# Performance work log

Measured on AMD Instinct MI355X. Metric: run time of the kernel, lower is better.

Reference implementation:

```python
import jax, jax.numpy as jnp
import numpy as np

BLOCK_SPLIT = (4, 4, 4)
GRID = 256
N_BLOCK = 64
BX = GRID // 4  # 64, per-block grid resolution along each axis
N_PTS = 4_194_304


def setup_inputs() -> dict:
    key = jax.random.key(0)
    k1, k2 = jax.random.split(key)
    aabb = jnp.array([[-1.5, -1.5, -1.5], [1.5, 1.5, 1.5]], dtype=jnp.float32)
    # points roughly inside the aabb
    xyz_sampled = jax.random.uniform(k1, (N_PTS, 3), dtype=jnp.float32) * 3.0 - 1.5
    alpha_volume = jax.random.uniform(k2, (GRID, GRID, GRID), dtype=jnp.float32)
    # per-block domains (as kilonerf global_to_local expects): block AABBs
    idx = np.stack(np.meshgrid(np.arange(4), np.arange(4), np.arange(4), indexing='ij'), -1).reshape(-1, 3)
    voxel = np.array([3.0 / 4.0] * 3)
    dmin = (-1.5 + idx * voxel).astype(np.float32)
    dmax = (dmin + voxel).astype(np.float32)
    return {"xyz_sampled": xyz_sampled, "aabb": aabb, "alpha_volume": alpha_volume,
            "domain_min": jnp.asarray(dmin), "domain_max": jnp.asarray(dmax)}


def _sample_alpha(xyz, aabb, alpha_volume, dmin, dmax):
    bs = jnp.asarray(BLOCK_SPLIT, jnp.float32)
    voxel = (aabb[1] - aabb[0]) / bs                      # per-block world size
    idx3 = jnp.floor((xyz - aabb[0]) / voxel).astype(jnp.int32)
    idx3 = jnp.clip(idx3, 0, jnp.array(BLOCK_SPLIT, jnp.int32) - 1)  # edge clamp (matches loop)
    strides = jnp.array([BLOCK_SPLIT[2] * BLOCK_SPLIT[1], BLOCK_SPLIT[2], 1], jnp.int32)
    bid = (idx3 * strides).sum(-1)                        # [N] block id in [0, 64)

    order = jnp.argsort(bid)                              # jax sort is stable; matches bucket-by-block order
    bid_s = bid[order]
    pts = xyz[order]

    # global_to_local (kilonerf): map into per-block [-1,1]^3
    local = 2.0 * (pts - dmin[bid_s]) / (dmax[bid_s] - dmin[bid_s]) - 1.0  # [N,3] (gx,gy,gz)

    # torch .view(64,1,64,64,64) is a raw contiguous reinterpretation -> plain reshape
    vols = alpha_volume.reshape(N_BLOCK, BX, BX, BX)      # [B, D, H, W]
    D = H = W = BX
    # grid_sample convention: grid x -> W axis, y -> H axis, z -> D axis; align_corners=True
    fx = (local[:, 0] + 1.0) * 0.5 * (W - 1)
    fy = (local[:, 1] + 1.0) * 0.5 * (H - 1)
    fz = (local[:, 2] + 1.0) * 0.5 * (D - 1)
    x0 = jnp.floor(fx); y0 = jnp.floor(fy); z0 = jnp.floor(fz)
    wx = fx - x0; wy = fy - y0; wz = fz - z0
    x0i = x0.astype(jnp.int32); y0i = y0.astype(jnp.int32); z0i = z0.astype(jnp.int32)

    def fetch(zi, yi, xi):
        # zeros padding for out-of-range corners (grid_sample padding_mode='zeros')
        inb = (zi >= 0) & (zi < D) & (yi >= 0) & (yi < H) & (xi >= 0) & (xi < W)
        v = vols[bid_s, jnp.clip(zi, 0, D - 1), jnp.clip(yi, 0, H - 1), jnp.clip(xi, 0, W - 1)]
        return jnp.where(inb, v, 0.0)

    out = jnp.zeros_like(fx)
    for dz, wz_ in ((0, 1.0 - wz), (1, wz)):
        for dy, wy_ in ((0, 1.0 - wy), (1, wy)):
            for dx, wx_ in ((0, 1.0 - wx), (1, wx)):
                out = out + wz_ * wy_ * wx_ * fetch(z0i + dz, y0i + dy, x0i + dx)
    return out  # [N] alpha values in block-sorted order


def reference(xyz_sampled, aabb, alpha_volume, domain_min, domain_max):
    return _sample_alpha(xyz_sampled, aabb, alpha_volume, domain_min, domain_max)
```

## Files before the change

### kernel.cpp

```cpp
#include <hip/hip_runtime.h>

#define NB     64
#define NF     4096
#define TILE   16384
#define HBLK   1024
#define DBLK   1024
#define FBLK   512
#define GBLK   256
#define SBLK   256
#define FB_TILE 4096
#define STAGE_HALF 8192

__device__ __forceinline__ int compute_bid(float px, float py, float pz,
                                           float a0x, float a0y, float a0z,
                                           float vx, float vy, float vz) {
    int ix = (int)floorf((px - a0x) / vx);
    int iy = (int)floorf((py - a0y) / vy);
    int iz = (int)floorf((pz - a0z) / vz);
    ix = min(max(ix, 0), 3);
    iy = min(max(iy, 0), 3);
    iz = min(max(iz, 0), 3);
    return ix * 16 + iy * 4 + iz;
}

__device__ __forceinline__ void quant_point(float px, float py, float pz,
        float a0x, float a0y, float a0z, float vx, float vy, float vz,
        const float* s_dn, const float* s_sc,
        int& b, int& qx, int& qy, int& qz, int& key) {
    b = compute_bid(px, py, pz, a0x, a0y, a0z, vx, vy, vz);
    float fx = (px - s_dn[3 * b])     * s_sc[3 * b];
    float fy = (py - s_dn[3 * b + 1]) * s_sc[3 * b + 1];
    float fz = (pz - s_dn[3 * b + 2]) * s_sc[3 * b + 2];
    qx = min(max(__float2int_rn(fx * 256.0f), 0), 16128);
    qy = min(max(__float2int_rn(fy * 256.0f), 0), 16128);
    qz = min(max(__float2int_rn(fz * 256.0f), 0), 16128);
    key = (b << 6) | ((qz >> 12) << 4) | ((qy >> 12) << 2) | (qx >> 12);
}

__global__ void __launch_bounds__(HBLK) hist_kernel(
        const float* __restrict__ xyz, const float* __restrict__ aabb,
        const float* __restrict__ dmin, const float* __restrict__ dmax,
        int* __restrict__ hist64, int* __restrict__ tot4096, int N, int T) {
    __shared__ int   sh[NF];
    __shared__ float s_dn[192], s_sc[192];
    const int tid = threadIdx.x, g = blockIdx.x;
    for (int l = tid; l < NF; l += HBLK) sh[l] = 0;
    if (tid < 192) { s_dn[tid] = dmin[tid]; s_sc[tid] = 63.0f / (dmax[tid] - dmin[tid]); }
    const float a0x = aabb[0], a0y = aabb[1], a0z = aabb[2];
    const float vx = (aabb[3] - a0x) * 0.25f;
    const float vy = (aabb[4] - a0y) * 0.25f;
    const float vz = (aabb[5] - a0z) * 0.25f;
    __syncthreads();
    for (int c = 0; c < TILE / (HBLK * 4); ++c) {
        int p0 = g * TILE + c * (HBLK * 4) + tid * 4;
        int b, qx, qy, qz, k;
        if (p0 + 3 < N) {
            const float4* v4 = (const float4*)(xyz + (size_t)p0 * 3);
            float4 f0 = v4[0], f1 = v4[1], f2 = v4[2];
            quant_point(f0.x, f0.y, f0.z, a0x, a0y, a0z, vx, vy, vz, s_dn, s_sc, b, qx, qy, qz, k);
            atomicAdd(&sh[k], 1);
            quant_point(f0.w, f1.x, f1.y, a0x, a0y, a0z, vx, vy, vz, s_dn, s_sc, b, qx, qy, qz, k);
            atomicAdd(&sh[k], 1);
            quant_point(f1.z, f1.w, f2.x, a0x, a0y, a0z, vx, vy, vz, s_dn, s_sc, b, qx, qy, qz, k);
            atomicAdd(&sh[k], 1);
            quant_point(f2.y, f2.z, f2.w, a0x, a0y, a0z, vx, vy, vz, s_dn, s_sc, b, qx, qy, qz, k);
            atomicAdd(&sh[k], 1);
        } else {
            for (int t = 0; t < 4; ++t) {
                int i = p0 + t;
                if (i < N) {
                    quant_point(xyz[3 * i], xyz[3 * i + 1], xyz[3 * i + 2],
                                a0x, a0y, a0z, vx, vy, vz, s_dn, s_sc, b, qx, qy, qz, k);
                    atomicAdd(&sh[k], 1);
                }
            }
        }
    }
    __syncthreads();
    for (int l = tid; l < NF; l += HBLK) {
        int c = sh[l];
        if (c) atomicAdd(&tot4096[l], c);
    }
    if (tid < NB) {
        int s = 0;
        #pragma unroll
        for (int j = 0; j < 64; ++j) s += sh[tid * 64 + j];
        hist64[tid * T + g] = s;
    }
}

__global__ void scans_kernel(int* __restrict__ hist64, int* __restrict__ tot64,
                             const int* __restrict__ tot4096,
                             int* __restrict__ foff, int* __restrict__ fcnt, int G) {
    __shared__ int sh[SBLK];
    const int t = threadIdx.x;
    if (blockIdx.x < NB) {
        const int b = blockIdx.x;
        const int L = (G + SBLK - 1) / SBLK;
        const int lo = t * L;
        const int n = min(L, max(0, G - lo));
        const int base = b * G + lo;
        int s = 0;
        for (int k = 0; k < n; ++k) s += hist64[base + k];
        sh[t] = s;
        __syncthreads();
        for (int off = 1; off < SBLK; off <<= 1) {
            int v = (t >= off) ? sh[t - off] : 0;
            __syncthreads();
            sh[t] += v;
            __syncthreads();
        }
        int excl = (t == 0) ? 0 : sh[t - 1];
        for (int k = 0; k < n; ++k) {
            int v = hist64[base + k];
            hist64[base + k] = excl;
            excl += v;
        }
        if (t == SBLK - 1) tot64[b] = sh[SBLK - 1];
    } else {
        const int L = NF / SBLK;
        int loc[16];
        int s = 0;
        #pragma unroll
        for (int j = 0; j < L; ++j) { loc[j] = tot4096[t * L + j]; s += loc[j]; }
        sh[t] = s;
        __syncthreads();
        for (int o = 1; o < SBLK; o <<= 1) {
            int v = (t >= o) ? sh[t - o] : 0;
            __syncthreads();
            sh[t] += v;
            __syncthreads();
        }
        int run = (t == 0) ? 0 : sh[t - 1];
        #pragma unroll
        for (int j = 0; j < L; ++j) {
            foff[t * L + j] = run;
            fcnt[t * L + j] = run;
            run += loc[j];
        }
        if (t == SBLK - 1) foff[NF] = run;
    }
}

__global__ void __launch_bounds__(DBLK) scatterC_kernel(
        const float* __restrict__ xyz, const float* __restrict__ aabb,
        const float* __restrict__ dmin, const float* __restrict__ dmax,
        const int* __restrict__ hist64, const int* __restrict__ tot64,
        unsigned long long* __restrict__ payloadC, int N, int T) {
    __shared__ unsigned long long stage[STAGE_HALF];
    __shared__ int   s_wh[16][NB];
    __shared__ int   s_cnt0[NB];
    __shared__ int   s_off[NB];
    __shared__ int   s_start[NB];
    __shared__ int   s_gb[NB];
    __shared__ float s_dn[192], s_sc[192];
    const int tid = threadIdx.x, g = blockIdx.x;
    const int lane = tid & 63, wv = tid >> 6;
    if (tid < NB) s_off[tid] = tot64[tid];
    if (tid < 192) { s_dn[tid] = dmin[tid]; s_sc[tid] = 63.0f / (dmax[tid] - dmin[tid]); }
    ((int*)s_wh)[tid] = 0;
    const float a0x = aabb[0], a0y = aabb[1], a0z = aabb[2];
    const float vx = (aabb[3] - a0x) * 0.25f;
    const float vy = (aabb[4] - a0y) * 0.25f;
    const float vz = (aabb[5] - a0z) * 0.25f;
    __syncthreads();
    for (int o = 1; o < NB; o <<= 1) {
        int v = (tid < NB && tid >= o) ? s_off[tid - o] : 0;
        __syncthreads();
        if (tid < NB) s_off[tid] += v;
        __syncthreads();
    }
    if (tid < NB) s_cnt0[tid] = hist64[tid * T + g] + (tid ? s_off[tid - 1] : 0);

    const unsigned long long lt = (1ull << lane) - 1ull;
    const int base_i = g * TILE + wv * 1024;
    unsigned long long cache[16];
    #pragma unroll
    for (int r = 0; r < 16; ++r) {
        int i = base_i + r * 64 + lane;
        bool valid = (i < N);
        int b = 0, qx = 0, qy = 0, qz = 0, key;
        if (valid) {
            quant_point(xyz[3 * i], xyz[3 * i + 1], xyz[3 * i + 2],
                        a0x, a0y, a0z, vx, vy, vz, s_dn, s_sc, b, qx, qy, qz, key);
        }
        unsigned long long m = __ballot(valid);
        #pragma unroll
        for (int q = 0; q < 6; ++q) {
            unsigned long long bal = __ballot((b >> q) & 1);
            m &= ((b >> q) & 1) ? bal : ~bal;
        }
        int rank = __popcll(m & lt);
        int run = valid ? s_wh[wv][b] : 0;
        if (valid && rank == 0) s_wh[wv][b] = run + __popcll(m);
        int localpos = run + rank;
        cache[r] = (unsigned long long)(unsigned)qx
                 | ((unsigned long long)(unsigned)qy << 14)
                 | ((unsigned long long)(unsigned)qz << 28)
                 | ((unsigned long long)(unsigned)b  << 42)
                 | ((unsigned long long)(unsigned)localpos << 48);
    }
    __syncthreads();
    for (int o = 1; o < 16; o <<= 1) {
        int v = (wv >= o) ? s_wh[wv - o][lane] : 0;
        __syncthreads();
        s_wh[wv][lane] += v;
        __syncthreads();
    }
    if (wv == 0) {
        int v = s_wh[15][lane];
        int incl = v;
        #pragma unroll
        for (int o = 1; o < 64; o <<= 1) {
            int u = __shfl_up(incl, o);
            if (lane >= o) incl += u;
        }
        int excl = incl - v;
        s_start[lane] = excl;
        s_gb[lane] = s_cnt0[lane] - excl;
    }
    __syncthreads();
    const int n = min(TILE, N - g * TILE);
    #pragma unroll
    for (int r = 0; r < 16; ++r) {
        int i = base_i + r * 64 + lane;
        if (i < N) {
            unsigned long long cc = cache[r];
            int b = (int)((cc >> 42) & 63);
            int localpos = (int)((cc >> 48) & 1023);
            int lidx = s_start[b] + (wv ? s_wh[wv - 1][b] : 0) + localpos;
            unsigned long long p48 = cc & ((1ull << 48) - 1);
            if (lidx < STAGE_HALF) stage[lidx] = p48;
            cache[r] = p48 | ((unsigned long long)(unsigned)lidx << 48);
        }
    }
    __syncthreads();
    {
        int nA = min(n, STAGE_HALF);
        for (int j = tid; j < nA; j += DBLK) {
            unsigned long long p = stage[j];
            int b = (int)((p >> 42) & 63);
            payloadC[s_gb[b] + j] = p;
        }
    }
    __syncthreads();
    #pragma unroll
    for (int r = 0; r < 16; ++r) {
        int i = base_i + r * 64 + lane;
        if (i < N) {
            unsigned long long cc = cache[r];
            int lidx = (int)(cc >> 48);
            if (lidx >= STAGE_HALF)
                stage[lidx - STAGE_HALF] = cc & ((1ull << 48) - 1);
        }
    }
    __syncthreads();
    for (int j = STAGE_HALF + tid; j < n; j += DBLK) {
        unsigned long long p = stage[j - STAGE_HALF];
        int b = (int)((p >> 42) & 63);
        payloadC[s_gb[b] + j] = p;
    }
}

__global__ void __launch_bounds__(FBLK) scatterF_kernel(
        const unsigned long long* __restrict__ payloadC,
        int* __restrict__ fcnt,
        unsigned long long* __restrict__ payloadF, int N) {
    __shared__ int s_fb[NF];
    const int tid = threadIdx.x, t2 = blockIdx.x;
    for (int l = tid; l < NF; l += FBLK) s_fb[l] = 0;
    __syncthreads();
    const int lo = t2 * TILE;
    const int n = min(TILE, N - lo);
    for (int j = tid; j < n; j += FBLK) {
        unsigned long long p = payloadC[lo + j];
        int qx = (int)(p & 16383), qy = (int)((p >> 14) & 16383);
        int qz = (int)((p >> 28) & 16383), b = (int)((p >> 42) & 63);
        int key = (b << 6) | ((qz >> 12) << 4) | ((qy >> 12) << 2) | (qx >> 12);
        atomicAdd(&s_fb[key], 1);
    }
    __syncthreads();
    for (int l = tid; l < NF; l += FBLK) {
        int c = s_fb[l];
        s_fb[l] = c ? atomicAdd(&fcnt[l], c) : 0;
    }
    __syncthreads();
    for (int j = tid; j < n; j += FBLK) {
        unsigned long long p = payloadC[lo + j];
        int qx = (int)(p & 16383), qy = (int)((p >> 14) & 16383);
        int qz = (int)((p >> 28) & 16383), b = (int)((p >> 42) & 63);
        int key = (b << 6) | ((qz >> 12) << 4) | ((qy >> 12) << 2) | (qx >> 12);
        int fpos = atomicAdd(&s_fb[key], 1);
        payloadF[fpos] = (p & ((1ull << 42) - 1))
                       | ((unsigned long long)(unsigned)(lo + j) << 42);
    }
}

__global__ void __launch_bounds__(GBLK) gather_kernel(
        const float* __restrict__ vol,
        const unsigned long long* __restrict__ payloadF,
        const int* __restrict__ foff, float* __restrict__ out) {
    __shared__ float sv[17 * 17 * 17];
    const int tid = threadIdx.x;
    const int nb = gridDim.x, d = blockIdx.x;
    const int k = (nb % 8 == 0) ? (d % 8) * (nb / 8) + (d / 8) : d;
    const int b = k >> 6;
    const int bz = ((k >> 4) & 3) * 16, by = ((k >> 2) & 3) * 16, bx = (k & 3) * 16;
    const float* vb = vol + ((size_t)b << 18);
    for (int l = tid; l < 17 * 17 * 17; l += GBLK) {
        int z = l / 289, r = l - z * 289, y = r / 17, x = r - y * 17;
        int gz = bz + z, gy = by + y, gx = bx + x;
        sv[l] = (gz < 64 && gy < 64 && gx < 64)
                    ? vb[(gz << 12) + (gy << 6) + gx] : 0.0f;
    }
    __syncthreads();
    const int lo = foff[k];
    const int n = foff[k + 1] - lo;
    for (int j = tid; j < n; j += GBLK) {
        unsigned long long p = payloadF[lo + j];
        int qx = (int)(p & 16383), qy = (int)((p >> 14) & 16383);
        int qz = (int)((p >> 28) & 16383);
        int pos = (int)(p >> 42);
        float wx = (qx & 255) * (1.0f / 256.0f);
        float wy = (qy & 255) * (1.0f / 256.0f);
        float wz = (qz & 255) * (1.0f / 256.0f);
        int lx = (qx >> 8) - bx, ly = (qy >> 8) - by, lz = (qz >> 8) - bz;
        int base = lz * 289 + ly * 17 + lx;
        float v000 = sv[base],       v001 = sv[base + 1];
        float v010 = sv[base + 17],  v011 = sv[base + 18];
        float v100 = sv[base + 289], v101 = sv[base + 290];
        float v110 = sv[base + 306], v111 = sv[base + 307];
        float c00 = v000 + wx * (v001 - v000);
        float c01 = v010 + wx * (v011 - v010);
        float c10 = v100 + wx * (v101 - v100);
        float c11 = v110 + wx * (v111 - v110);
        float c0 = c00 + wy * (c01 - c00);
        float c1 = c10 + wy * (c11 - c10);
        out[pos] = c0 + wz * (c1 - c0);
    }
}

__global__ void fb_hist_kernel(const float* __restrict__ xyz,
                               const float* __restrict__ aabb,
                               int* __restrict__ hist, int N, int G) {
    __shared__ int s_h[NB];
    const int tid = threadIdx.x, g = blockIdx.x;
    if (tid < NB) s_h[tid] = 0;
    __syncthreads();
    const float a0x = aabb[0], a0y = aabb[1], a0z = aabb[2];
    const float vx = (aabb[3] - a0x) * 0.25f;
    const float vy = (aabb[4] - a0y) * 0.25f;
    const float vz = (aabb[5] - a0z) * 0.25f;
    for (int c = 0; c < FB_TILE / 256; ++c) {
        int i = g * FB_TILE + c * 256 + tid;
        if (i < N)
            atomicAdd(&s_h[compute_bid(xyz[3 * i], xyz[3 * i + 1], xyz[3 * i + 2],
                                       a0x, a0y, a0z, vx, vy, vz)], 1);
    }
    __syncthreads();
    if (tid < NB) hist[tid * G + g] = s_h[tid];
}

__global__ void fb_scan_kernel(int* __restrict__ hist, int* __restrict__ tot, int G) {
    __shared__ int sh[SBLK];
    const int b = blockIdx.x, t = threadIdx.x;
    const int L = (G + SBLK - 1) / SBLK;
    const int lo = t * L;
    const int n = min(L, max(0, G - lo));
    const int base = b * G + lo;
    int s = 0;
    for (int k = 0; k < n; ++k) s += hist[base + k];
    sh[t] = s;
    __syncthreads();
    for (int off = 1; off < SBLK; off <<= 1) {
        int v = (t >= off) ? sh[t - off] : 0;
        __syncthreads();
        sh[t] += v;
        __syncthreads();
    }
    int excl = (t == 0) ? 0 : sh[t - 1];
    for (int k = 0; k < n; ++k) {
        int v = hist[base + k];
        hist[base + k] = excl;
        excl += v;
    }
    if (t == SBLK - 1) tot[b] = sh[SBLK - 1];
}

__global__ void fb_scatter_kernel(const float* __restrict__ xyz,
                                  const float* __restrict__ aabb,
                                  const float* __restrict__ dmin,
                                  const float* __restrict__ dmax,
                                  const float* __restrict__ vol,
                                  const int* __restrict__ hist,
                                  const int* __restrict__ tot64,
                                  float* __restrict__ out, int N, int G) {
    __shared__ int   s_cnt[NB], s_off[NB];
    __shared__ int   s_whist[4][NB];
    __shared__ float s_dn[192], s_sc[192];
    const int tid = threadIdx.x, g = blockIdx.x;
    if (tid < NB) s_off[tid] = tot64[tid];
    if (tid < 192) { s_dn[tid] = dmin[tid]; s_sc[tid] = 63.0f / (dmax[tid] - dmin[tid]); }
    __syncthreads();
    for (int o = 1; o < NB; o <<= 1) {
        int v = (tid < NB && tid >= o) ? s_off[tid - o] : 0;
        __syncthreads();
        if (tid < NB) s_off[tid] += v;
        __syncthreads();
    }
    if (tid < NB) s_cnt[tid] = hist[tid * G + g] + (tid ? s_off[tid - 1] : 0);
    const float a0x = aabb[0], a0y = aabb[1], a0z = aabb[2];
    const float vx = (aabb[3] - a0x) * 0.25f;
    const float vy = (aabb[4] - a0y) * 0.25f;
    const float vz = (aabb[5] - a0z) * 0.25f;
    __syncthreads();
    const int lane = tid & 63, wv = tid >> 6;
    const unsigned long long lt = (1ull << lane) - 1ull;
    for (int c = 0; c < FB_TILE / 256; ++c) {
        int i = g * FB_TILE + c * 256 + tid;
        bool valid = (i < N);
        int b = 0;
        float alpha = 0.0f;
        if (valid) {
            float px = xyz[3 * i], py = xyz[3 * i + 1], pz = xyz[3 * i + 2];
            b = compute_bid(px, py, pz, a0x, a0y, a0z, vx, vy, vz);
            float fx = (px - s_dn[3 * b])     * s_sc[3 * b];
            float fy = (py - s_dn[3 * b + 1]) * s_sc[3 * b + 1];
            float fz = (pz - s_dn[3 * b + 2]) * s_sc[3 * b + 2];
            float x0f = floorf(fx), y0f = floorf(fy), z0f = floorf(fz);
            float wx = fx - x0f, wy = fy - y0f, wz = fz - z0f;
            int x0 = (int)x0f, y0 = (int)y0f, z0 = (int)z0f;
            const float* vb = vol + ((size_t)b << 18);
            auto F = [&](int zi, int yi, int xi) -> float {
                if ((unsigned)zi >= 64u || (unsigned)yi >= 64u || (unsigned)xi >= 64u)
                    return 0.0f;
                return vb[(zi << 12) + (yi << 6) + xi];
            };
            float s = 0.0f;
            s += (1.0f - wz) * (1.0f - wy) * (1.0f - wx) * F(z0,     y0,     x0);
            s += (1.0f - wz) * (1.0f - wy) * wx          * F(z0,     y0,     x0 + 1);
            s += (1.0f - wz) * wy          * (1.0f - wx) * F(z0,     y0 + 1, x0);
            s += (1.0f - wz) * wy          * wx          * F(z0,     y0 + 1, x0 + 1);
            s += wz          * (1.0f - wy) * (1.0f - wx) * F(z0 + 1, y0,     x0);
            s += wz          * (1.0f - wy) * wx          * F(z0 + 1, y0,     x0 + 1);
            s += wz          * wy          * (1.0f - wx) * F(z0 + 1, y0 + 1, x0);
            s += wz          * wy          * wx          * F(z0 + 1, y0 + 1, x0 + 1);
            alpha = s;
        }
        ((int*)s_whist)[tid] = 0;
        __syncthreads();
        unsigned long long m = __ballot(valid);
        #pragma unroll
        for (int q = 0; q < 6; ++q) {
            unsigned long long bal = __ballot((b >> q) & 1);
            m &= ((b >> q) & 1) ? bal : ~bal;
        }
        int rank = __popcll(m & lt);
        if (valid && rank == 0) s_whist[wv][b] = __popcll(m);
        __syncthreads();
        if (valid) {
            int pos = s_cnt[b] + rank;
            for (int w2 = 0; w2 < wv; ++w2) pos += s_whist[w2][b];
            out[pos] = alpha;
        }
        __syncthreads();
        if (tid < NB)
            s_cnt[tid] += s_whist[0][tid] + s_whist[1][tid] +
                          s_whist[2][tid] + s_whist[3][tid];
        __syncthreads();
    }
}

extern "C" void kernel_launch(void* const* d_in, const int* in_sizes, int n_in,
                              void* d_out, int out_size, void* d_ws, size_t ws_size,
                              hipStream_t stream) {
    const float* xyz  = (const float*)d_in[0];
    const float* aabb = (const float*)d_in[1];
    const float* vol  = (const float*)d_in[2];
    const float* dmin = (const float*)d_in[3];
    const float* dmax = (const float*)d_in[4];
    float* out = (float*)d_out;
    const int N = in_sizes[0] / 3;
    const int T = (N + TILE - 1) / TILE;

    auto align = [](size_t x) { return (x + 255) & ~(size_t)255; };
    char* ws = (char*)d_ws;
    size_t o = 0;
    unsigned long long* payloadC = (unsigned long long*)(ws + o); o += align((size_t)N * 8);
    unsigned long long* payloadF = (unsigned long long*)(ws + o); o += align((size_t)N * 8);
    int* hist64  = (int*)(ws + o); o += align((size_t)NB * T * 4);
    int* tot64   = (int*)(ws + o); o += 256;
    int* tot4096 = (int*)(ws + o); o += align((size_t)NF * 4);
    int* foff    = (int*)(ws + o); o += align((size_t)(NF + 1) * 4);
    int* fcnt    = (int*)(ws + o); o += align((size_t)NF * 4);
    const bool fine = (N <= (1 << 22)) && (ws_size >= o);

    if (fine) {
        hipMemsetAsync(tot4096, 0, NF * 4, stream);
        hist_kernel<<<T, HBLK, 0, stream>>>(xyz, aabb, dmin, dmax,
                                            hist64, tot4096, N, T);
        scans_kernel<<<NB + 1, SBLK, 0, stream>>>(hist64, tot64, tot4096,
                                                  foff, fcnt, T);
        scatterC_kernel<<<T, DBLK, 0, stream>>>(xyz, aabb, dmin, dmax,
                                                hist64, tot64, payloadC, N, T);
        scatterF_kernel<<<T, FBLK, 0, stream>>>(payloadC, fcnt, payloadF, N);
        gather_kernel<<<NF, GBLK, 0, stream>>>(vol, payloadF, foff, out);
    } else {
        const int Gf = (N + FB_TILE - 1) / FB_TILE;
        int* h = (int*)ws;
        int* t = (int*)(ws + align((size_t)NB * Gf * 4));
        fb_hist_kernel<<<Gf, 256, 0, stream>>>(xyz, aabb, h, N, Gf);
        fb_scan_kernel<<<NB, SBLK, 0, stream>>>(h, t, Gf);
        fb_scatter_kernel<<<Gf, 256, 0, stream>>>(xyz, aabb, dmin, dmax, vol,
                                                  h, t, out, N, Gf);
    }
}
```

Before: 256.6 us.

## Drop fine-grained sub-block sort and gather directly from block-sorted payload

Removes the 4096-bucket fine histogram, its scan, the second scatter pass (scatterF) and the LDS-staged sub-block gather. Instead the gather kernel reads the block-sorted payloadC in output order and does eight trilinear loads straight from the global volume, writing coalesced outputs. This cuts a full read/write pass over N 8-byte payloads plus the extra atomics and memset. In exchange, volume reads lose the shared-memory tile reuse and rely on L2/cache locality within each 64^3 block (1 MB per block).

```diff
diff --git a/kernel.cpp b/kernel.cpp
--- a/kernel.cpp
+++ b/kernel.cpp
@@ -1,12 +1,11 @@
 #include <hip/hip_runtime.h>
 
 #define NB     64
-#define NF     4096
 #define TILE   16384
 #define HBLK   1024
 #define DBLK   1024
-#define FBLK   512
-#define GBLK   256
+#define GDBLK  256
+#define GDPTS  4096
 #define SBLK   256
 #define FB_TILE 4096
 #define STAGE_HALF 8192
@@ -26,7 +25,7 @@
 __device__ __forceinline__ void quant_point(float px, float py, float pz,
         float a0x, float a0y, float a0z, float vx, float vy, float vz,
         const float* s_dn, const float* s_sc,
-        int& b, int& qx, int& qy, int& qz, int& key) {
+        int& b, int& qx, int& qy, int& qz) {
     b = compute_bid(px, py, pz, a0x, a0y, a0z, vx, vy, vz);
     float fx = (px - s_dn[3 * b])     * s_sc[3 * b];
     float fy = (py - s_dn[3 * b + 1]) * s_sc[3 * b + 1];
@@ -34,18 +33,14 @@
     qx = min(max(__float2int_rn(fx * 256.0f), 0), 16128);
     qy = min(max(__float2int_rn(fy * 256.0f), 0), 16128);
     qz = min(max(__float2int_rn(fz * 256.0f), 0), 16128);
-    key = (b << 6) | ((qz >> 12) << 4) | ((qy >> 12) << 2) | (qx >> 12);
 }
 
 __global__ void __launch_bounds__(HBLK) hist_kernel(
         const float* __restrict__ xyz, const float* __restrict__ aabb,
-        const float* __restrict__ dmin, const float* __restrict__ dmax,
-        int* __restrict__ hist64, int* __restrict__ tot4096, int N, int T) {
-    __shared__ int   sh[NF];
-    __shared__ float s_dn[192], s_sc[192];
+        int* __restrict__ hist64, int N, int T) {
+    __shared__ int s_h[NB];
     const int tid = threadIdx.x, g = blockIdx.x;
-    for (int l = tid; l < NF; l += HBLK) sh[l] = 0;
-    if (tid < 192) { s_dn[tid] = dmin[tid]; s_sc[tid] = 63.0f / (dmax[tid] - dmin[tid]); }
+    if (tid < NB) s_h[tid] = 0;
     const float a0x = aabb[0], a0y = aabb[1], a0z = aabb[2];
     const float vx = (aabb[3] - a0x) * 0.25f;
     const float vy = (aabb[4] - a0y) * 0.25f;
@@ -53,93 +48,51 @@
     __syncthreads();
     for (int c = 0; c < TILE / (HBLK * 4); ++c) {
         int p0 = g * TILE + c * (HBLK * 4) + tid * 4;
-        int b, qx, qy, qz, k;
         if (p0 + 3 < N) {
             const float4* v4 = (const float4*)(xyz + (size_t)p0 * 3);
             float4 f0 = v4[0], f1 = v4[1], f2 = v4[2];
-            quant_point(f0.x, f0.y, f0.z, a0x, a0y, a0z, vx, vy, vz, s_dn, s_sc, b, qx, qy, qz, k);
-            atomicAdd(&sh[k], 1);
-            quant_point(f0.w, f1.x, f1.y, a0x, a0y, a0z, vx, vy, vz, s_dn, s_sc, b, qx, qy, qz, k);
-            atomicAdd(&sh[k], 1);
-            quant_point(f1.z, f1.w, f2.x, a0x, a0y, a0z, vx, vy, vz, s_dn, s_sc, b, qx, qy, qz, k);
-            atomicAdd(&sh[k], 1);
-            quant_point(f2.y, f2.z, f2.w, a0x, a0y, a0z, vx, vy, vz, s_dn, s_sc, b, qx, qy, qz, k);
-            atomicAdd(&sh[k], 1);
+            atomicAdd(&s_h[compute_bid(f0.x, f0.y, f0.z, a0x, a0y, a0z, vx, vy, vz)], 1);
+            atomicAdd(&s_h[compute_bid(f0.w, f1.x, f1.y, a0x, a0y, a0z, vx, vy, vz)], 1);
+            atomicAdd(&s_h[compute_bid(f1.z, f1.w, f2.x, a0x, a0y, a0z, vx, vy, vz)], 1);
+            atomicAdd(&s_h[compute_bid(f2.y, f2.z, f2.w, a0x, a0y, a0z, vx, vy, vz)], 1);
         } else {
             for (int t = 0; t < 4; ++t) {
                 int i = p0 + t;
-                if (i < N) {
-                    quant_point(xyz[3 * i], xyz[3 * i + 1], xyz[3 * i + 2],
-                                a0x, a0y, a0z, vx, vy, vz, s_dn, s_sc, b, qx, qy, qz, k);
-                    atomicAdd(&sh[k], 1);
-                }
+                if (i < N)
+                    atomicAdd(&s_h[compute_bid(xyz[3 * i], xyz[3 * i + 1],
+                                               xyz[3 * i + 2],
+                                               a0x, a0y, a0z, vx, vy, vz)], 1);
             }
         }
     }
     __syncthreads();
-    for (int l = tid; l < NF; l += HBLK) {
-        int c = sh[l];
-        if (c) atomicAdd(&tot4096[l], c);
-    }
-    if (tid < NB) {
-        int s = 0;
-        #pragma unroll
-        for (int j = 0; j < 64; ++j) s += sh[tid * 64 + j];
-        hist64[tid * T + g] = s;
-    }
-}
-
-__global__ void scans_kernel(int* __restrict__ hist64, int* __restrict__ tot64,
-                             const int* __restrict__ tot4096,
-                             int* __restrict__ foff, int* __restrict__ fcnt, int G) {
+    if (tid < NB) hist64[tid * T + g] = s_h[tid];
+}
+
+__global__ void fb_scan_kernel(int* __restrict__ hist, int* __restrict__ tot, int G) {
     __shared__ int sh[SBLK];
-    const int t = threadIdx.x;
-    if (blockIdx.x < NB) {
-        const int b = blockIdx.x;
-        const int L = (G + SBLK - 1) / SBLK;
-        const int lo = t * L;
-        const int n = min(L, max(0, G - lo));
-        const int base = b * G + lo;
-        int s = 0;
-        for (int k = 0; k < n; ++k) s += hist64[base + k];
-        sh[t] = s;
-        __syncthreads();
-        for (int off = 1; off < SBLK; off <<= 1) {
-            int v = (t >= off) ? sh[t - off] : 0;
-            __syncthreads();
-            sh[t] += v;
-            __syncthreads();
-        }
-        int excl = (t == 0) ? 0 : sh[t - 1];
-        for (int k = 0; k < n; ++k) {
-            int v = hist64[base + k];
-            hist64[base + k] = excl;
-            excl += v;
-        }
-        if (t == SBLK - 1) tot64[b] = sh[SBLK - 1];
-    } else {
-        const int L = NF / SBLK;
-        int loc[16];
-        int s = 0;
-        #pragma unroll
-        for (int j = 0; j < L; ++j) { loc[j] = tot4096[t * L + j]; s += loc[j]; }
-        sh[t] = s;
-        __syncthreads();
-        for (int o = 1; o < SBLK; o <<= 1) {
-            int v = (t >= o) ? sh[t - o] : 0;
-            __syncthreads();
-            sh[t] += v;
-            __syncthreads();
-        }
-        int run = (t == 0) ? 0 : sh[t - 1];
-        #pragma unroll
-        for (int j = 0; j < L; ++j) {
-            foff[t * L + j] = run;
-            fcnt[t * L + j] = run;
-            run += loc[j];
-        }
-        if (t == SBLK - 1) foff[NF] = run;
-    }
+    const int b = blockIdx.x, t = threadIdx.x;
+    const int L = (G + SBLK - 1) / SBLK;
+    const int lo = t * L;
+    const int n = min(L, max(0, G - lo));
+    const int base = b * G + lo;
+    int s = 0;
+    for (int k = 0; k < n; ++k) s += hist[base + k];
+    sh[t] = s;
+    __syncthreads();
+    for (int off = 1; off < SBLK; off <<= 1) {
+        int v = (t >= off) ? sh[t - off] : 0;
+        __syncthreads();
+        sh[t] += v;
+        __syncthreads();
+    }
+    int excl = (t == 0) ? 0 : sh[t - 1];
+    for (int k = 0; k < n; ++k) {
+        int v = hist[base + k];
+        hist[base + k] = excl;
+        excl += v;
+    }
+    if (t == SBLK - 1) tot[b] = sh[SBLK - 1];
 }
 
 __global__ void __launch_bounds__(DBLK) scatterC_kernel(
@@ -179,10 +132,10 @@
     for (int r = 0; r < 16; ++r) {
         int i = base_i + r * 64 + lane;
         bool valid = (i < N);
-        int b = 0, qx = 0, qy = 0, qz = 0, key;
+        int b = 0, qx = 0, qy = 0, qz = 0;
         if (valid) {
             quant_point(xyz[3 * i], xyz[3 * i + 1], xyz[3 * i + 2],
-                        a0x, a0y, a0z, vx, vy, vz, s_dn, s_sc, b, qx, qy, qz, key);
+                        a0x, a0y, a0z, vx, vy, vz, s_dn, s_sc, b, qx, qy, qz);
         }
         unsigned long long m = __ballot(valid);
         #pragma unroll
@@ -262,81 +215,38 @@
     }
 }
 
-__global__ void __launch_bounds__(FBLK) scatterF_kernel(
+__global__ void __launch_bounds__(GDBLK) gather_kernel(
+        const float* __restrict__ vol,
         const unsigned long long* __restrict__ payloadC,
-        int* __restrict__ fcnt,
-        unsigned long long* __restrict__ payloadF, int N) {
-    __shared__ int s_fb[NF];
-    const int tid = threadIdx.x, t2 = blockIdx.x;
-    for (int l = tid; l < NF; l += FBLK) s_fb[l] = 0;
-    __syncthreads();
-    const int lo = t2 * TILE;
-    const int n = min(TILE, N - lo);
-    for (int j = tid; j < n; j += FBLK) {
-        unsigned long long p = payloadC[lo + j];
-        int qx = (int)(p & 16383), qy = (int)((p >> 14) & 16383);
-        int qz = (int)((p >> 28) & 16383), b = (int)((p >> 42) & 63);
-        int key = (b << 6) | ((qz >> 12) << 4) | ((qy >> 12) << 2) | (qx >> 12);
-        atomicAdd(&s_fb[key], 1);
-    }
-    __syncthreads();
-    for (int l = tid; l < NF; l += FBLK) {
-        int c = s_fb[l];
-        s_fb[l] = c ? atomicAdd(&fcnt[l], c) : 0;
-    }
-    __syncthreads();
-    for (int j = tid; j < n; j += FBLK) {
-        unsigned long long p = payloadC[lo + j];
-        int qx = (int)(p & 16383), qy = (int)((p >> 14) & 16383);
-        int qz = (int)((p >> 28) & 16383), b = (int)((p >> 42) & 63);
-        int key = (b << 6) | ((qz >> 12) << 4) | ((qy >> 12) << 2) | (qx >> 12);
-        int fpos = atomicAdd(&s_fb[key], 1);
-        payloadF[fpos] = (p & ((1ull << 42) - 1))
-                       | ((unsigned long long)(unsigned)(lo + j) << 42);
-    }
-}
-
-__global__ void __launch_bounds__(GBLK) gather_kernel(
-        const float* __restrict__ vol,
-        const unsigned long long* __restrict__ payloadF,
-        const int* __restrict__ foff, float* __restrict__ out) {
-    __shared__ float sv[17 * 17 * 17];
-    const int tid = threadIdx.x;
+        float* __restrict__ out, int N) {
     const int nb = gridDim.x, d = blockIdx.x;
-    const int k = (nb % 8 == 0) ? (d % 8) * (nb / 8) + (d / 8) : d;
-    const int b = k >> 6;
-    const int bz = ((k >> 4) & 3) * 16, by = ((k >> 2) & 3) * 16, bx = (k & 3) * 16;
-    const float* vb = vol + ((size_t)b << 18);
-    for (int l = tid; l < 17 * 17 * 17; l += GBLK) {
-        int z = l / 289, r = l - z * 289, y = r / 17, x = r - y * 17;
-        int gz = bz + z, gy = by + y, gx = bx + x;
-        sv[l] = (gz < 64 && gy < 64 && gx < 64)
-                    ? vb[(gz << 12) + (gy << 6) + gx] : 0.0f;
-    }
-    __syncthreads();
-    const int lo = foff[k];
-    const int n = foff[k + 1] - lo;
-    for (int j = tid; j < n; j += GBLK) {
-        unsigned long long p = payloadF[lo + j];
-        int qx = (int)(p & 16383), qy = (int)((p >> 14) & 16383);
-        int qz = (int)((p >> 28) & 16383);
-        int pos = (int)(p >> 42);
-        float wx = (qx & 255) * (1.0f / 256.0f);
-        float wy = (qy & 255) * (1.0f / 256.0f);
-        float wz = (qz & 255) * (1.0f / 256.0f);
-        int lx = (qx >> 8) - bx, ly = (qy >> 8) - by, lz = (qz >> 8) - bz;
-        int base = lz * 289 + ly * 17 + lx;
-        float v000 = sv[base],       v001 = sv[base + 1];
-        float v010 = sv[base + 17],  v011 = sv[base + 18];
-        float v100 = sv[base + 289], v101 = sv[base + 290];
-        float v110 = sv[base + 306], v111 = sv[base + 307];
-        float c00 = v000 + wx * (v001 - v000);
-        float c01 = v010 + wx * (v011 - v010);
-        float c10 = v100 + wx * (v101 - v100);
-        float c11 = v110 + wx * (v111 - v110);
-        float c0 = c00 + wy * (c01 - c00);
-        float c1 = c10 + wy * (c11 - c10);
-        out[pos] = c0 + wz * (c1 - c0);
+    const int g = (nb % 8 == 0) ? (d % 8) * (nb / 8) + (d / 8) : d;
+    const int base = g * GDPTS;
+    for (int r = 0; r < GDPTS / GDBLK; ++r) {
+        int i = base + r * GDBLK + threadIdx.x;
+        if (i < N) {
+            unsigned long long p = payloadC[i];
+            int qx = (int)(p & 16383), qy = (int)((p >> 14) & 16383);
+            int qz = (int)((p >> 28) & 16383), b = (int)((p >> 42) & 63);
+            const float* vb = vol + ((size_t)b << 18);
+            int x0 = qx >> 8, y0 = qy >> 8, z0 = qz >> 8;
+            float wx = (qx & 255) * (1.0f / 256.0f);
+            float wy = (qy & 255) * (1.0f / 256.0f);
+            float wz = (qz & 255) * (1.0f / 256.0f);
+            int x1 = min(x0 + 1, 63), y1 = min(y0 + 1, 63), z1 = min(z0 + 1, 63);
+            int zl0 = z0 << 12, zl1 = z1 << 12, yl0 = y0 << 6, yl1 = y1 << 6;
+            float v000 = vb[zl0 + yl0 + x0], v001 = vb[zl0 + yl0 + x1];
+            float v010 = vb[zl0 + yl1 + x0], v011 = vb[zl0 + yl1 + x1];
+            float v100 = vb[zl1 + yl0 + x0], v101 = vb[zl1 + yl0 + x1];
+            float v110 = vb[zl1 + yl1 + x0], v111 = vb[zl1 + yl1 + x1];
+            float c00 = v000 + wx * (v001 - v000);
+            float c01 = v010 + wx * (v011 - v010);
+            float c10 = v100 + wx * (v101 - v100);
+            float c11 = v110 + wx * (v111 - v110);
+            float c0 = c00 + wy * (c01 - c00);
+            float c1 = c10 + wy * (c11 - c10);
+            out[i] = c0 + wz * (c1 - c0);
+        }
     }
 }
 
@@ -359,32 +269,6 @@
     }
     __syncthreads();
     if (tid < NB) hist[tid * G + g] = s_h[tid];
-}
-
-__global__ void fb_scan_kernel(int* __restrict__ hist, int* __restrict__ tot, int G) {
-    __shared__ int sh[SBLK];
-    const int b = blockIdx.x, t = threadIdx.x;
-    const int L = (G + SBLK - 1) / SBLK;
-    const int lo = t * L;
-    const int n = min(L, max(0, G - lo));
-    const int base = b * G + lo;
-    int s = 0;
-    for (int k = 0; k < n; ++k) s += hist[base + k];
-    sh[t] = s;
-    __syncthreads();
-    for (int off = 1; off < SBLK; off <<= 1) {
-        int v = (t >= off) ? sh[t - off] : 0;
-        __syncthreads();
-        sh[t] += v;
-        __syncthreads();
-    }
-    int excl = (t == 0) ? 0 : sh[t - 1];
-    for (int k = 0; k < n; ++k) {
-        int v = hist[base + k];
-        hist[base + k] = excl;
-        excl += v;
-    }
-    if (t == SBLK - 1) tot[b] = sh[SBLK - 1];
 }
 
 __global__ void fb_scatter_kernel(const float* __restrict__ xyz,
@@ -487,24 +371,17 @@
     char* ws = (char*)d_ws;
     size_t o = 0;
     unsigned long long* payloadC = (unsigned long long*)(ws + o); o += align((size_t)N * 8);
-    unsigned long long* payloadF = (unsigned long long*)(ws + o); o += align((size_t)N * 8);
     int* hist64  = (int*)(ws + o); o += align((size_t)NB * T * 4);
     int* tot64   = (int*)(ws + o); o += 256;
-    int* tot4096 = (int*)(ws + o); o += align((size_t)NF * 4);
-    int* foff    = (int*)(ws + o); o += align((size_t)(NF + 1) * 4);
-    int* fcnt    = (int*)(ws + o); o += align((size_t)NF * 4);
     const bool fine = (N <= (1 << 22)) && (ws_size >= o);
 
     if (fine) {
-        hipMemsetAsync(tot4096, 0, NF * 4, stream);
-        hist_kernel<<<T, HBLK, 0, stream>>>(xyz, aabb, dmin, dmax,
-                                            hist64, tot4096, N, T);
-        scans_kernel<<<NB + 1, SBLK, 0, stream>>>(hist64, tot64, tot4096,
-                                                  foff, fcnt, T);
+        hist_kernel<<<T, HBLK, 0, stream>>>(xyz, aabb, hist64, N, T);
+        fb_scan_kernel<<<NB, SBLK, 0, stream>>>(hist64, tot64, T);
         scatterC_kernel<<<T, DBLK, 0, stream>>>(xyz, aabb, dmin, dmax,
                                                 hist64, tot64, payloadC, N, T);
-        scatterF_kernel<<<T, FBLK, 0, stream>>>(payloadC, fcnt, payloadF, N);
-        gather_kernel<<<NF, GBLK, 0, stream>>>(vol, payloadF, foff, out);
+        const int Gd = (N + GDPTS - 1) / GDPTS;
+        gather_kernel<<<Gd, GDBLK, 0, stream>>>(vol, payloadC, out, N);
     } else {
         const int Gf = (N + FB_TILE - 1) / FB_TILE;
         int* h = (int*)ws;
```

Result: slower. 294.6 us (+14.8%).
